# Optimization experiments

Hardware: AMD Instinct MI355X
Metric: run time of the kernel (lower is better)

Reference implementation:

```python
import jax, jax.numpy as jnp
import numpy as np

B, N_PTS, M_ROIS = 2, 8192, 2048
C_IN, O, H, NS = 128, 256, 4, 32
RADIUS = 1.6
BN_EPS = 1e-5
SCALE = 10.0  # point cloud extent


def setup_inputs() -> dict:
    key = jax.random.key(0)
    ks = jax.random.split(key, 20)
    f32 = jnp.float32
    Cg = C_IN + 3  # grouper concats relative xyz to features

    def kaiming(k, shape, fan_in):
        return jax.random.normal(k, shape, f32) * np.sqrt(2.0 / fan_in)

    inp = {
        "xyz": jax.random.uniform(ks[0], (B, N_PTS, 3), f32) * SCALE,
        "new_xyz": jax.random.uniform(ks[1], (B, M_ROIS, 3), f32) * SCALE,
        "features": jax.random.normal(ks[2], (B, C_IN, N_PTS), f32),
        # conv1d (kernel=1, no bias) weights, torch layout (out, in)
        "pos_w": kaiming(ks[3], (O, 3), 3),
        "key_w": kaiming(ks[4], (O, Cg), Cg),
        "val_w1": kaiming(ks[5], (O, Cg), Cg),
        "bn1_g": jnp.ones((O,), f32), "bn1_b": jnp.zeros((O,), f32),
        "val_w2": kaiming(ks[6], (O, O), O),
        "bn2_g": jnp.ones((O,), f32), "bn2_b": jnp.zeros((O,), f32),
        "attn_w": kaiming(ks[7], (H, O), O),
        # sigmoid-gated coefficient linears (no bias)
        "kc_w": kaiming(ks[8], (O, O), O),
        "qc_w": kaiming(ks[9], (O, O), O),
        "qkc_w": kaiming(ks[10], (O, O), O),
        "vc_w": kaiming(ks[11], (O, O), O),
        # cls/reg weight MLPs: Linear(O,O//2)+ReLU, Linear(O//2,1)+Sigmoid
        "cls_w1": kaiming(ks[12], (O // 2, O), O), "cls_b1": jnp.zeros((O // 2,), f32),
        "cls_w2": kaiming(ks[13], (1, O // 2), O // 2), "cls_b2": jnp.zeros((1,), f32),
        "reg_w1": kaiming(ks[14], (O // 2, O), O), "reg_b1": jnp.zeros((O // 2,), f32),
        "reg_w2": kaiming(ks[15], (1, O // 2), O // 2), "reg_b2": jnp.zeros((1,), f32),
    }
    return inp


def _bn(x, g, b):
    # eval-mode BatchNorm1d with running_mean=0, running_var=1 (init state)
    return g[None, :, None] * (x * (1.0 / np.sqrt(1.0 + BN_EPS))) + b[None, :, None]


def _conv1x1(w, x):  # (O,C) x (M,C,NS) -> (M,O,NS)
    return jnp.einsum('oc,mcn->mon', w, x)


def _ball_group(pts, q):
    # ball query: first NS points within RADIUS of each query (pad with first hit)
    n_tot = pts.shape[0]
    d2 = jnp.sum((q[:, None, :] - pts[None, :, :]) ** 2, axis=-1)  # (M, Ntot)
    order = jnp.where(d2 < RADIUS ** 2, jnp.arange(n_tot, dtype=jnp.int32), n_tot)
    neg_vals, idx = jax.lax.top_k(-order, NS)  # smallest indices among in-ball pts
    valid = (-neg_vals) < n_tot
    idx = jnp.where(valid, idx, idx[:, :1])  # pad with first neighbor
    has_any = valid[:, :1]
    idx = jnp.where(has_any, idx, 0)  # empty balls -> point 0
    return idx, ~has_any[:, 0]


def reference(xyz, new_xyz, features, pos_w, key_w, val_w1, bn1_g, bn1_b,
              val_w2, bn2_g, bn2_b, attn_w, kc_w, qc_w, qkc_w, vc_w,
              cls_w1, cls_b1, cls_w2, cls_b2, reg_w1, reg_b1, reg_w2, reg_b2):
    pts = xyz.reshape(-1, 3)                                   # (Ntot, 3)
    feats = features.transpose(0, 2, 1).reshape(-1, C_IN)      # (Ntot, C)
    q = new_xyz.reshape(-1, 3)                                 # (M, 3)

    idx, empty_mask = _ball_group(pts, q)                      # (M, NS)
    gx = pts[idx] - q[:, None, :]                              # relative xyz (M,NS,3)
    gxt = gx.transpose(0, 2, 1)                                # (M,3,NS)
    gf = jnp.concatenate([gx, feats[idx]], axis=-1).transpose(0, 2, 1)  # (M,C+3,NS)

    pos = jax.nn.relu(_conv1x1(pos_w, gxt))                    # (M,O,NS)
    key = jax.nn.relu(_conv1x1(key_w, gf))                     # (M,O,NS)
    v = jax.nn.relu(_bn(_conv1x1(val_w1, gf), bn1_g, bn1_b))
    val = jax.nn.relu(_bn(_conv1x1(val_w2, v), bn2_g, bn2_b))  # (M,O,NS)
    pos_key = pos * key

    sig = jax.nn.sigmoid
    v_c = sig(pos.mean(2) @ vc_w.T)                            # (M,O)
    q_c = sig(pos.mean(2) @ qc_w.T)
    k_c = sig(key.mean(2) @ kc_w.T)
    qk_c = sig(pos_key.mean(2) @ qkc_w.T)

    val = val + pos * v_c[:, :, None]
    attn_emb = pos * q_c[:, :, None] + key * k_c[:, :, None] + pos_key * qk_c[:, :, None]
    attn = jax.nn.softmax(jnp.einsum('ho,mon->mhn', attn_w, attn_emb), axis=-1)  # (M,H,NS)

    m = val.shape[0]
    vh = val.reshape(m, H, O // H, NS)
    new_features = jnp.einsum('mhdn,mhn->mhd', vh, attn).reshape(m, O)  # (M,O)

    def gate(x, w1, b1, w2, b2):
        return sig(jax.nn.relu(x @ w1.T + b1) @ w2.T + b2)

    cls_features = new_features * gate(new_features, cls_w1, cls_b1, cls_w2, cls_b2)
    reg_features = new_features * gate(new_features, reg_w1, reg_b1, reg_w2, reg_b2)
    return new_features, cls_features, reg_features
```

## Files before the change

kernel.cpp:

```cpp
#include <hip/hip_runtime.h>

#define DI __device__ __forceinline__

typedef __attribute__((ext_vector_type(8))) short bf16x8;
typedef __attribute__((ext_vector_type(4))) short s16x4;
typedef __attribute__((ext_vector_type(4))) float f32x4;

DI short f2bs(float x){ unsigned u = __float_as_uint(x);
  return (short)((u + 0x7FFF + ((u >> 16) & 1)) >> 16); }
DI float bs2f(short s){ return __uint_as_float(((unsigned)(unsigned short)s) << 16); }
DI f32x4 MFMA(bf16x8 a, bf16x8 b, f32x4 c){
  return __builtin_amdgcn_mfma_f32_16x16x32_bf16(a, b, c, 0, 0, 0);
}

constexpr int NP   = 8192;
constexpr int NTOT = 16384;
constexpr int M    = 4096;
constexpr int C    = 128;
constexpr int O    = 256;
constexpr int NS   = 32;
constexpr int H    = 4;
constexpr int GFS  = 136;
constexpr int VS   = 264;
constexpr float BNS = 0.99999500003749969f;

DI void copy64(short* __restrict__ dst, const short* __restrict__ src, int t){
  int row = t >> 2, off = (t & 3) * 64;
  const short* sp = src + row*VS + off;
  short* dp = dst + (size_t)row*O + off;
  #pragma unroll
  for(int j = 0; j < 8; j++)
    *(bf16x8*)(dp + j*8) = *(const bf16x8*)(sp + j*8);
}

__global__ __launch_bounds__(256) void k_transpose(const float* __restrict__ feat,
                                                   short* __restrict__ fT){
  __shared__ float tile[128][65];
  int blk = blockIdx.x;
  int b  = blk >> 7;
  int n0 = (blk & 127) << 6;
  int t = threadIdx.x;
  int nn = t & 63, c4 = t >> 6;
  const float* src = feat + (size_t)b * C * NP;
  for(int i = 0; i < 32; i++){
    int c = c4 * 32 + i;
    tile[c][nn] = src[(size_t)c * NP + n0 + nn];
  }
  __syncthreads();
  int c2 = t & 127, nb = t >> 7;
  for(int j = 0; j < 32; j++){
    int n = nb + j * 2;
    fT[((size_t)(b * NP + n0 + n)) * C + c2] = f2bs(tile[c2][n]);
  }
}

__global__ __launch_bounds__(256) void k_pack(
    const float* __restrict__ kw, const float* __restrict__ v1w,
    const float* __restrict__ v2w, const float* __restrict__ pw,
    const float* __restrict__ vcw, const float* __restrict__ qcw,
    const float* __restrict__ kcw, const float* __restrict__ qkcw,
    const float* __restrict__ cw1, const float* __restrict__ rw1,
    short* __restrict__ keyP, short* __restrict__ v1P,
    float* __restrict__ kgx, float* __restrict__ v1gx, float* __restrict__ pgx,
    short* __restrict__ v2b,
    short* __restrict__ gw,
    short* __restrict__ cw1b, short* __restrict__ rw1b)
{
  int i = blockIdx.x * 256 + threadIdx.x;
  if(i < O * C){
    int o = i >> 7, k = i & 127;
    keyP[i] = f2bs(kw[o*131 + 3 + k]);
    v1P[i]  = f2bs(v1w[o*131 + 3 + k]);
  }
  if(i < O){
    for(int j = 0; j < 3; j++){
      kgx [i*4+j] = kw [i*131 + j];
      v1gx[i*4+j] = v1w[i*131 + j];
      pgx [i*4+j] = pw [i*3 + j];
    }
    kgx[i*4+3] = 0.0f; v1gx[i*4+3] = 0.0f; pgx[i*4+3] = 0.0f;
  }
  if(i < O * O){
    v2b[i] = f2bs(v2w[i]);
    gw[0*O*O + i] = f2bs(vcw[i]);
    gw[1*O*O + i] = f2bs(qcw[i]);
    gw[2*O*O + i] = f2bs(kcw[i]);
    gw[3*O*O + i] = f2bs(qkcw[i]);
  }
  if(i < (O/2) * O){
    cw1b[i] = f2bs(cw1[i]);
    rw1b[i] = f2bs(rw1[i]);
  }
}

__global__ __launch_bounds__(64) void k_ballq(const float* __restrict__ xyz,
                                              const float* __restrict__ nxyz,
                                              int* __restrict__ idxo,
                                              float* __restrict__ gxo){
#pragma clang fp contract(off)
  int m = blockIdx.x;
  int lane = threadIdx.x;
  float qx = nxyz[m*3+0], qy = nxyz[m*3+1], qz = nxyz[m*3+2];
  __shared__ int sel[NS];
  int cnt = 0;
  for(int base = 0; base < NTOT; base += 64){
    int p = base + lane;
    float dx = qx - xyz[p*3+0], dy = qy - xyz[p*3+1], dz = qz - xyz[p*3+2];
    float d2 = dx*dx + dy*dy;
    d2 = d2 + dz*dz;
    bool pred = d2 < 2.56f;
    unsigned long long bal = __ballot(pred);
    if(pred){
      int pos = cnt + __popcll(bal & ((1ull << lane) - 1ull));
      if(pos < NS) sel[pos] = p;
    }
    cnt += __popcll(bal);
    if(cnt >= NS) break;
  }
  __syncthreads();
  if(lane < NS){
    int s = 0;
    if(cnt > 0) s = (lane < cnt) ? sel[lane] : sel[0];
    idxo[m*NS + lane] = s;
    gxo[(m*NS+lane)*3+0] = xyz[s*3+0] - qx;
    gxo[(m*NS+lane)*3+1] = xyz[s*3+1] - qy;
    gxo[(m*NS+lane)*3+2] = xyz[s*3+2] - qz;
  }
}

__global__ __launch_bounds__(256, 3) void k_conv(
    const short* __restrict__ fT,
    const short* __restrict__ keyP, const short* __restrict__ v1P,
    const float* __restrict__ kgx, const float* __restrict__ v1gx,
    const float* __restrict__ pgx,
    const short* __restrict__ v2b,
    const float* __restrict__ g1, const float* __restrict__ b1,
    const float* __restrict__ g2, const float* __restrict__ b2,
    const int* __restrict__ idxw, const float* __restrict__ gxw,
    short* __restrict__ keyo, short* __restrict__ valo,
    float* __restrict__ mPos, float* __restrict__ mKey, float* __restrict__ mPK,
    int q0)
{
  int lq2 = blockIdx.x, t = threadIdx.x;
  int w = t >> 6, l = t & 63;
  int col = l & 15, kq = l >> 4;
  int ro = w * 64;
  __shared__ __align__(16) short gf[64 * GFS];
  __shared__ __align__(16) short vst[64 * VS];
  __shared__ float gxs[64 * 4];
  __shared__ int  sel[64];
  int qg0 = q0 + lq2 * 2;
  if(t < 64){
    int qi = t >> 5, n = t & 31;
    int gq = qg0 + qi;
    sel[t] = idxw[gq*NS + n];
    gxs[t*4+0] = gxw[(gq*NS+n)*3+0];
    gxs[t*4+1] = gxw[(gq*NS+n)*3+1];
    gxs[t*4+2] = gxw[(gq*NS+n)*3+2];
    gxs[t*4+3] = 0.0f;
  }
  __syncthreads();
  for(int i = 0; i < 16; i++){
    int n = w*16 + i;
    int p = sel[n];
    *(unsigned*)&gf[n*GFS + l*2] = *(const unsigned*)(fT + (size_t)p * C + l*2);
  }
  __syncthreads();

  f32x4 acc[4][4];
  const f32x4 vzero = {0.0f, 0.0f, 0.0f, 0.0f};

  for(int mt=0;mt<4;mt++) for(int nt=0;nt<4;nt++) acc[mt][nt] = vzero;
  for(int ks = 0; ks < 4; ks++){
    bf16x8 bf[4];
    for(int nt=0;nt<4;nt++)
      bf[nt] = *(const bf16x8*)&gf[(nt*16+col)*GFS + ks*32 + kq*8];
    for(int mt = 0; mt < 4; mt++){
      bf16x8 a = *(const bf16x8*)(keyP + (size_t)(ro + mt*16 + col)*C + ks*32 + kq*8);
      for(int nt=0;nt<4;nt++) acc[mt][nt] = MFMA(a, bf[nt], acc[mt][nt]);
    }
  }
  for(int mt=0;mt<4;mt++){
    int o0 = ro + mt*16 + kq*4;
    f32x4 kg[4], pg[4];
    for(int r=0;r<4;r++){ kg[r] = *(const f32x4*)(kgx + (o0+r)*4);
                          pg[r] = *(const f32x4*)(pgx + (o0+r)*4); }
    for(int qi=0; qi<2; qi++){
      float sp[4]={0,0,0,0}, sk[4]={0,0,0,0}, spk[4]={0,0,0,0};
      for(int h=0; h<2; h++){
        int nt = qi*2 + h;
        int n  = nt*16 + col;
        float gx0 = gxs[n*4+0], gx1 = gxs[n*4+1], gx2 = gxs[n*4+2];
        s16x4 pk;
        for(int r=0;r<4;r++){
          float kk = fmaxf(acc[mt][nt][r] + kg[r][0]*gx0 + kg[r][1]*gx1 + kg[r][2]*gx2, 0.0f);
          float pv = fmaxf(pg[r][0]*gx0 + pg[r][1]*gx1 + pg[r][2]*gx2, 0.0f);
          pk[r] = f2bs(kk);
          sp[r] += pv; sk[r] += kk; spk[r] += pv*kk;
        }
        *(s16x4*)&vst[n*VS + o0] = pk;
      }
      for(int r=0;r<4;r++){
        float a = sp[r], b = sk[r], c = spk[r];
        for(int msk=1; msk<16; msk<<=1){
          a += __shfl_xor(a, msk); b += __shfl_xor(b, msk); c += __shfl_xor(c, msk);
        }
        if(col == 0){
          int lql = lq2*2 + qi;
          mPos[(size_t)lql*O + o0 + r] = a * 0.03125f;
          mKey[(size_t)lql*O + o0 + r] = b * 0.03125f;
          mPK [(size_t)lql*O + o0 + r] = c * 0.03125f;
        }
      }
    }
  }
  __syncthreads();
  copy64(keyo + (size_t)lq2*64*O, vst, t);

  for(int mt=0;mt<4;mt++) for(int nt=0;nt<4;nt++) acc[mt][nt] = vzero;
  for(int ks = 0; ks < 4; ks++){
    bf16x8 bf[4];
    for(int nt=0;nt<4;nt++)
      bf[nt] = *(const bf16x8*)&gf[(nt*16+col)*GFS + ks*32 + kq*8];
    for(int mt = 0; mt < 4; mt++){
      bf16x8 a = *(const bf16x8*)(v1P + (size_t)(ro + mt*16 + col)*C + ks*32 + kq*8);
      for(int nt=0;nt<4;nt++) acc[mt][nt] = MFMA(a, bf[nt], acc[mt][nt]);
    }
  }
  __syncthreads();
  for(int mt=0;mt<4;mt++){
    int o0 = ro + mt*16 + kq*4;
    f32x4 vg[4];
    float gg[4], bb[4];
    for(int r=0;r<4;r++){ vg[r] = *(const f32x4*)(v1gx + (o0+r)*4);
                          gg[r] = g1[o0+r]; bb[r] = b1[o0+r]; }
    for(int nt=0;nt<4;nt++){
      int n = nt*16 + col;
      float gx0 = gxs[n*4+0], gx1 = gxs[n*4+1], gx2 = gxs[n*4+2];
      s16x4 pk;
      for(int r=0;r<4;r++){
        float x = acc[mt][nt][r] + vg[r][0]*gx0 + vg[r][1]*gx1 + vg[r][2]*gx2;
        pk[r] = f2bs(fmaxf(gg[r]*(x * BNS) + bb[r], 0.0f));
      }
      *(s16x4*)&vst[n*VS + o0] = pk;
    }
  }
  __syncthreads();

  for(int mt=0;mt<4;mt++) for(int nt=0;nt<4;nt++) acc[mt][nt] = vzero;
  for(int ks = 0; ks < 8; ks++){
    bf16x8 bf[4];
    for(int nt=0;nt<4;nt++)
      bf[nt] = *(const bf16x8*)&vst[(nt*16+col)*VS + ks*32 + kq*8];
    for(int mt = 0; mt < 4; mt++){
      bf16x8 a = *(const bf16x8*)(v2b + (size_t)(ro + mt*16 + col)*O + ks*32 + kq*8);
      for(int nt=0;nt<4;nt++) acc[mt][nt] = MFMA(a, bf[nt], acc[mt][nt]);
    }
  }
  s16x4 valS[4][4];
  for(int mt=0;mt<4;mt++){
    int o0 = ro + mt*16 + kq*4;
    float gg[4], bb[4];
    for(int r=0;r<4;r++){ gg[r] = g2[o0+r]; bb[r] = b2[o0+r]; }
    for(int nt=0;nt<4;nt++)
      for(int r=0;r<4;r++)
        valS[mt][nt][r] = f2bs(fmaxf(gg[r]*(acc[mt][nt][r] * BNS) + bb[r], 0.0f));
  }
  __syncthreads();
  for(int mt=0;mt<4;mt++) for(int nt=0;nt<4;nt++){
    int n = nt*16 + col;
    *(s16x4*)&vst[n*VS + ro + mt*16 + kq*4] = valS[mt][nt];
  }
  __syncthreads();
  copy64(valo + (size_t)lq2*64*O, vst, t);
}

__global__ __launch_bounds__(256) void k_gates(
    const float* __restrict__ mPos, const float* __restrict__ mKey,
    const float* __restrict__ mPK, const short* __restrict__ gw,
    float* __restrict__ gates)
{
  int t = threadIdx.x, w = t >> 6, l = t & 63, col = l & 15, kq = l >> 4;
  int lq0 = blockIdx.x * 16;
  const float* A  = (w < 2) ? mPos : ((w == 2) ? mKey : mPK);
  const short* Wg = gw + (size_t)w * O * O;
  f32x4 acc[16];
  const f32x4 vzero = {0.0f,0.0f,0.0f,0.0f};
  for(int i=0;i<16;i++) acc[i] = vzero;
  for(int ks = 0; ks < 8; ks++){
    union { bf16x8 v; short e[8]; } u;
    const float* ap = A + (size_t)(lq0 + col)*O + ks*32 + kq*8;
    for(int j = 0; j < 8; j++) u.e[j] = f2bs(ap[j]);
    for(int nt = 0; nt < 16; nt++){
      bf16x8 bv = *(const bf16x8*)(Wg + (size_t)(nt*16 + col)*O + ks*32 + kq*8);
      acc[nt] = MFMA(u.v, bv, acc[nt]);
    }
  }
  for(int nt=0;nt<16;nt++) for(int r=0;r<4;r++){
    int lqq = lq0 + kq*4 + r;
    int oo = nt*16 + col;
    gates[((size_t)lqq*4 + w)*O + oo] = 1.0f / (1.0f + expf(-acc[nt][r]));
  }
}

__global__ __launch_bounds__(256) void k_attn(
    const short* __restrict__ keyw, const short* __restrict__ valw,
    const float* __restrict__ gxw, const float* __restrict__ posw,
    const float* __restrict__ attw, const float* __restrict__ gates,
    float* __restrict__ outNF, int q0)
{
  int lq = blockIdx.x, q = q0 + lq, t = threadIdx.x;
  __shared__ float emL[O * 33];
  __shared__ float attnL[H * NS];
  __shared__ float gxs[NS * 3];
  __shared__ float partial[256];
  if(t < 96) gxs[t] = gxw[q*96 + t];
  float vc  = gates[((size_t)lq*4 + 0)*O + t];
  float qc  = gates[((size_t)lq*4 + 1)*O + t];
  float kc  = gates[((size_t)lq*4 + 2)*O + t];
  float qkc = gates[((size_t)lq*4 + 3)*O + t];
  float pw0 = posw[t*3+0], pw1 = posw[t*3+1], pw2 = posw[t*3+2];
  __syncthreads();
  float posr[NS];
  for(int n = 0; n < NS; n++)
    posr[n] = fmaxf(pw0*gxs[n*3] + pw1*gxs[n*3+1] + pw2*gxs[n*3+2], 0.0f);
  for(int n = 0; n < NS; n++){
    float k = bs2f(keyw[((size_t)lq*NS + n)*O + t]);
    emL[t*33 + n] = posr[n]*qc + k*kc + posr[n]*k*qkc;
  }
  __syncthreads();
  {
    int idx = t & 127, h = idx >> 5, n = idx & 31, half = t >> 7;
    float s = 0;
    const float* aw = attw + h*O + half*128;
    for(int o = 0; o < 128; o++) s += aw[o] * emL[(half*128 + o)*33 + n];
    partial[t] = s;
  }
  __syncthreads();
  if(t < 128){
    int h = t >> 5, n = t & 31;
    float s = partial[t] + partial[t + 128];
    float mx = s;
    for(int msk=1; msk<32; msk<<=1) mx = fmaxf(mx, __shfl_xor(mx, msk));
    float e = expf(s - mx);
    float sum = e;
    for(int msk=1; msk<32; msk<<=1) sum += __shfl_xor(sum, msk);
    attnL[h*NS + n] = e / sum;
  }
  __syncthreads();
  int h = t >> 6;
  float nf = 0;
  for(int n = 0; n < NS; n++){
    float v = bs2f(valw[((size_t)lq*NS + n)*O + t]);
    nf += (v + posr[n]*vc) * attnL[h*NS + n];
  }
  outNF[(size_t)q*O + t] = nf;
}

__global__ __launch_bounds__(256) void k_fgate(
    const float* __restrict__ nf,
    const short* __restrict__ cw1b, const float* __restrict__ cb1,
    const float* __restrict__ cw2, const float* __restrict__ cb2,
    const short* __restrict__ rw1b, const float* __restrict__ rb1,
    const float* __restrict__ rw2, const float* __restrict__ rb2,
    float* __restrict__ outC, float* __restrict__ outR)
{
  int t = threadIdx.x, w = t >> 6, l = t & 63, col = l & 15, kq = l >> 4;
  int q0 = blockIdx.x * 64;
  __shared__ float sC[64], sR[64];
  f32x4 acc[16];
  const f32x4 vzero = {0.0f,0.0f,0.0f,0.0f};
  for(int i=0;i<16;i++) acc[i] = vzero;
  int arow = q0 + w*16 + col;
  for(int ks = 0; ks < 8; ks++){
    union { bf16x8 v; short e[8]; } u;
    const float* ap = nf + (size_t)arow*O + ks*32 + kq*8;
    for(int j = 0; j < 8; j++) u.e[j] = f2bs(ap[j]);
    for(int nt = 0; nt < 16; nt++){
      const short* W1 = (nt < 8) ? cw1b : rw1b;
      int j = (nt & 7)*16 + col;
      bf16x8 bv = *(const bf16x8*)(W1 + (size_t)j*O + ks*32 + kq*8);
      acc[nt] = MFMA(u.v, bv, acc[nt]);
    }
  }
  for(int r = 0; r < 4; r++){
    float pc = 0, pr = 0;
    for(int nt = 0; nt < 8; nt++){
      int j = nt*16 + col;
      pc += fmaxf(acc[nt][r] + cb1[j], 0.0f) * cw2[j];
    }
    for(int nt = 8; nt < 16; nt++){
      int j = (nt - 8)*16 + col;
      pr += fmaxf(acc[nt][r] + rb1[j], 0.0f) * rw2[j];
    }
    for(int msk=1; msk<16; msk<<=1){ pc += __shfl_xor(pc, msk); pr += __shfl_xor(pr, msk); }
    if(col == 0){
      int qq = w*16 + kq*4 + r;
      sC[qq] = 1.0f / (1.0f + expf(-(pc + cb2[0])));
      sR[qq] = 1.0f / (1.0f + expf(-(pr + rb2[0])));
    }
  }
  __syncthreads();
  for(int qq = 0; qq < 64; qq++){
    float nv = nf[(size_t)(q0 + qq)*O + t];
    outC[(size_t)(q0 + qq)*O + t] = nv * sC[qq];
    outR[(size_t)(q0 + qq)*O + t] = nv * sR[qq];
  }
}

extern "C" void kernel_launch(void* const* d_in, const int* in_sizes, int n_in,
                              void* d_out, int out_size, void* d_ws, size_t ws_size,
                              hipStream_t stream)
{
  const float* xyz  = (const float*)d_in[0];
  const float* nxyz = (const float*)d_in[1];
  const float* feat = (const float*)d_in[2];
  const float* posw = (const float*)d_in[3];
  const float* keyw = (const float*)d_in[4];
  const float* v1w  = (const float*)d_in[5];
  const float* bn1g = (const float*)d_in[6];
  const float* bn1b = (const float*)d_in[7];
  const float* v2w  = (const float*)d_in[8];
  const float* bn2g = (const float*)d_in[9];
  const float* bn2b = (const float*)d_in[10];
  const float* attw = (const float*)d_in[11];
  const float* kcw  = (const float*)d_in[12];
  const float* qcw  = (const float*)d_in[13];
  const float* qkcw = (const float*)d_in[14];
  const float* vcw  = (const float*)d_in[15];
  const float* cw1  = (const float*)d_in[16];
  const float* cb1  = (const float*)d_in[17];
  const float* cw2  = (const float*)d_in[18];
  const float* cb2  = (const float*)d_in[19];
  const float* rw1  = (const float*)d_in[20];
  const float* rb1  = (const float*)d_in[21];
  const float* rw2  = (const float*)d_in[22];
  const float* rb2  = (const float*)d_in[23];

  const size_t fixedB = 12000000;
  const size_t perQ   = 40960;
  int Q = 64;
  for(int cand : {4096, 2048, 1024, 512, 256, 128}){
    if(fixedB + (size_t)cand*perQ <= ws_size){ Q = cand; break; }
  }

  char* p = (char*)d_ws;
  auto alloc = [&](size_t bytes){ char* r = p; p += (bytes + 255) & ~size_t(255); return r; };
  short* fT    = (short*)alloc((size_t)NTOT*C*2);
  short* keyP  = (short*)alloc((size_t)O*C*2);
  short* v1P   = (short*)alloc((size_t)O*C*2);
  float* kgx   = (float*)alloc((size_t)O*4*4);
  float* v1gx  = (float*)alloc((size_t)O*4*4);
  float* pgx   = (float*)alloc((size_t)O*4*4);
  short* v2b   = (short*)alloc((size_t)O*O*2);
  short* gw    = (short*)alloc((size_t)4*O*O*2);
  short* cw1b  = (short*)alloc((size_t)(O/2)*O*2);
  short* rw1b  = (short*)alloc((size_t)(O/2)*O*2);
  int*   idxw  = (int*)  alloc((size_t)M*NS*4);
  float* gxw   = (float*)alloc((size_t)M*NS*3*4);
  short* keyo  = (short*)alloc((size_t)Q*NS*O*2);
  short* valo  = (short*)alloc((size_t)Q*NS*O*2);
  float* mPos  = (float*)alloc((size_t)Q*O*4);
  float* mKey  = (float*)alloc((size_t)Q*O*4);
  float* mPK   = (float*)alloc((size_t)Q*O*4);
  float* gates = (float*)alloc((size_t)Q*4*O*4);

  float* outNF = (float*)d_out;
  float* outC  = outNF + (size_t)M*O;
  float* outR  = outC  + (size_t)M*O;

  k_transpose<<<256, 256, 0, stream>>>(feat, fT);
  k_pack     <<<256, 256, 0, stream>>>(keyw, v1w, v2w, posw, vcw, qcw, kcw, qkcw, cw1, rw1,
                                       keyP, v1P, kgx, v1gx, pgx, v2b, gw, cw1b, rw1b);
  k_ballq    <<<M,   64,  0, stream>>>(xyz, nxyz, idxw, gxw);
  for(int q0 = 0; q0 < M; q0 += Q){
    k_conv  <<<Q/2,  256, 0, stream>>>(fT, keyP, v1P, kgx, v1gx, pgx, v2b,
                                       bn1g, bn1b, bn2g, bn2b,
                                       idxw, gxw, keyo, valo, mPos, mKey, mPK, q0);
    k_gates <<<Q/16, 256, 0, stream>>>(mPos, mKey, mPK, gw, gates);
    k_attn  <<<Q,    256, 0, stream>>>(keyo, valo, gxw, posw, attw, gates, outNF, q0);
  }
  k_fgate   <<<M/64, 256, 0, stream>>>(outNF, cw1b, cb1, cw2, cb2, rw1b, rb1, rw2, rb2, outC, outR);
}
```

Baseline: 438.1 us.

## Fuse conv, gate, attention and output-gating stages into one per-query-pair kernel

Merges k_conv, k_gates, k_attn and k_fgate into a single kernel that processes two queries per block. Key activations stay in registers, and means, gates, attention scores and new features stay in shared memory, so the bf16 key/value intermediates and gate buffers are never written to or read from global memory. The value-1 conv is computed first so its output can reuse the staging buffer. The gate and final MLP matmuls now run with only 2 useful columns out of 16 per MFMA, which wastes matrix throughput, and occupancy drops to 2 blocks per CU because of higher register and LDS use.

Result: slower. 570.8 us (+30.3%).

```diff
diff --git a/kernel.cpp b/kernel.cpp
--- a/kernel.cpp
+++ b/kernel.cpp
@@ -19,19 +19,9 @@
 constexpr int C    = 128;
 constexpr int O    = 256;
 constexpr int NS   = 32;
-constexpr int H    = 4;
 constexpr int GFS  = 136;
 constexpr int VS   = 264;
 constexpr float BNS = 0.99999500003749969f;
-
-DI void copy64(short* __restrict__ dst, const short* __restrict__ src, int t){
-  int row = t >> 2, off = (t & 3) * 64;
-  const short* sp = src + row*VS + off;
-  short* dp = dst + (size_t)row*O + off;
-  #pragma unroll
-  for(int j = 0; j < 8; j++)
-    *(bf16x8*)(dp + j*8) = *(const bf16x8*)(sp + j*8);
-}
 
 __global__ __launch_bounds__(256) void k_transpose(const float* __restrict__ feat,
                                                    short* __restrict__ fT){
@@ -64,7 +54,7 @@
     float* __restrict__ kgx, float* __restrict__ v1gx, float* __restrict__ pgx,
     short* __restrict__ v2b,
     short* __restrict__ gw,
-    short* __restrict__ cw1b, short* __restrict__ rw1b)
+    short* __restrict__ fgw)
 {
   int i = blockIdx.x * 256 + threadIdx.x;
   if(i < O * C){
@@ -86,10 +76,7 @@
     gw[1*O*O + i] = f2bs(qcw[i]);
     gw[2*O*O + i] = f2bs(kcw[i]);
     gw[3*O*O + i] = f2bs(qkcw[i]);
-  }
-  if(i < (O/2) * O){
-    cw1b[i] = f2bs(cw1[i]);
-    rw1b[i] = f2bs(rw1[i]);
+    fgw[i] = f2bs(i < 128*O ? cw1[i] : rw1[i - 128*O]);
   }
 }
 
@@ -128,18 +115,21 @@
   }
 }
 
-__global__ __launch_bounds__(256, 3) void k_conv(
+__global__ __launch_bounds__(256, 2) void k_fused(
     const short* __restrict__ fT,
     const short* __restrict__ keyP, const short* __restrict__ v1P,
     const float* __restrict__ kgx, const float* __restrict__ v1gx,
     const float* __restrict__ pgx,
-    const short* __restrict__ v2b,
+    const short* __restrict__ v2b, const short* __restrict__ gw,
+    const short* __restrict__ fgw, const float* __restrict__ attw,
     const float* __restrict__ g1, const float* __restrict__ b1,
     const float* __restrict__ g2, const float* __restrict__ b2,
+    const float* __restrict__ cb1, const float* __restrict__ cw2,
+    const float* __restrict__ cb2,
+    const float* __restrict__ rb1, const float* __restrict__ rw2,
+    const float* __restrict__ rb2,
     const int* __restrict__ idxw, const float* __restrict__ gxw,
-    short* __restrict__ keyo, short* __restrict__ valo,
-    float* __restrict__ mPos, float* __restrict__ mKey, float* __restrict__ mPK,
-    int q0)
+    float* __restrict__ outNF, float* __restrict__ outC, float* __restrict__ outR)
 {
   int lq2 = blockIdx.x, t = threadIdx.x;
   int w = t >> 6, l = t & 63;
@@ -149,7 +139,14 @@
   __shared__ __align__(16) short vst[64 * VS];
   __shared__ float gxs[64 * 4];
   __shared__ int  sel[64];
-  int qg0 = q0 + lq2 * 2;
+  __shared__ float attwL[4 * O];
+  __shared__ float meanL[3][2][O];
+  __shared__ float gatesL[4][2][O];
+  __shared__ float scoreP[4][4][64];
+  __shared__ float attnL[4][2][NS];
+  __shared__ float nfL[2][O];
+  __shared__ float pgsum[4][2];
+  int qg0 = lq2 * 2;
   if(t < 64){
     int qi = t >> 5, n = t & 31;
     int gq = qg0 + qi;
@@ -159,6 +156,7 @@
     gxs[t*4+2] = gxw[(gq*NS+n)*3+2];
     gxs[t*4+3] = 0.0f;
   }
+  for(int i = t; i < 4*O; i += 256) attwL[i] = attw[i];
   __syncthreads();
   for(int i = 0; i < 16; i++){
     int n = w*16 + i;
@@ -167,244 +165,240 @@
   }
   __syncthreads();
 
-  f32x4 acc[4][4];
   const f32x4 vzero = {0.0f, 0.0f, 0.0f, 0.0f};
 
-  for(int mt=0;mt<4;mt++) for(int nt=0;nt<4;nt++) acc[mt][nt] = vzero;
-  for(int ks = 0; ks < 4; ks++){
-    bf16x8 bf[4];
-    for(int nt=0;nt<4;nt++)
-      bf[nt] = *(const bf16x8*)&gf[(nt*16+col)*GFS + ks*32 + kq*8];
-    for(int mt = 0; mt < 4; mt++){
-      bf16x8 a = *(const bf16x8*)(keyP + (size_t)(ro + mt*16 + col)*C + ks*32 + kq*8);
-      for(int nt=0;nt<4;nt++) acc[mt][nt] = MFMA(a, bf[nt], acc[mt][nt]);
-    }
-  }
-  for(int mt=0;mt<4;mt++){
-    int o0 = ro + mt*16 + kq*4;
-    f32x4 kg[4], pg[4];
-    for(int r=0;r<4;r++){ kg[r] = *(const f32x4*)(kgx + (o0+r)*4);
-                          pg[r] = *(const f32x4*)(pgx + (o0+r)*4); }
-    for(int qi=0; qi<2; qi++){
-      float sp[4]={0,0,0,0}, sk[4]={0,0,0,0}, spk[4]={0,0,0,0};
-      for(int h=0; h<2; h++){
-        int nt = qi*2 + h;
-        int n  = nt*16 + col;
+  {
+    f32x4 acc[4][4];
+    for(int mt=0;mt<4;mt++) for(int nt=0;nt<4;nt++) acc[mt][nt] = vzero;
+    for(int ks = 0; ks < 4; ks++){
+      bf16x8 bf[4];
+      for(int nt=0;nt<4;nt++)
+        bf[nt] = *(const bf16x8*)&gf[(nt*16+col)*GFS + ks*32 + kq*8];
+      for(int mt = 0; mt < 4; mt++){
+        bf16x8 a = *(const bf16x8*)(v1P + (size_t)(ro + mt*16 + col)*C + ks*32 + kq*8);
+        for(int nt=0;nt<4;nt++) acc[mt][nt] = MFMA(a, bf[nt], acc[mt][nt]);
+      }
+    }
+    for(int mt=0;mt<4;mt++){
+      int o0 = ro + mt*16 + kq*4;
+      f32x4 vg[4];
+      float gg[4], bb[4];
+      for(int r=0;r<4;r++){ vg[r] = *(const f32x4*)(v1gx + (o0+r)*4);
+                            gg[r] = g1[o0+r]; bb[r] = b1[o0+r]; }
+      for(int nt=0;nt<4;nt++){
+        int n = nt*16 + col;
         float gx0 = gxs[n*4+0], gx1 = gxs[n*4+1], gx2 = gxs[n*4+2];
         s16x4 pk;
         for(int r=0;r<4;r++){
-          float kk = fmaxf(acc[mt][nt][r] + kg[r][0]*gx0 + kg[r][1]*gx1 + kg[r][2]*gx2, 0.0f);
-          float pv = fmaxf(pg[r][0]*gx0 + pg[r][1]*gx1 + pg[r][2]*gx2, 0.0f);
-          pk[r] = f2bs(kk);
-          sp[r] += pv; sk[r] += kk; spk[r] += pv*kk;
+          float x = acc[mt][nt][r] + vg[r][0]*gx0 + vg[r][1]*gx1 + vg[r][2]*gx2;
+          pk[r] = f2bs(fmaxf(gg[r]*(x * BNS) + bb[r], 0.0f));
         }
         *(s16x4*)&vst[n*VS + o0] = pk;
       }
+    }
+  }
+
+  f32x4 accK[4][4];
+  {
+    for(int mt=0;mt<4;mt++) for(int nt=0;nt<4;nt++) accK[mt][nt] = vzero;
+    for(int ks = 0; ks < 4; ks++){
+      bf16x8 bf[4];
+      for(int nt=0;nt<4;nt++)
+        bf[nt] = *(const bf16x8*)&gf[(nt*16+col)*GFS + ks*32 + kq*8];
+      for(int mt = 0; mt < 4; mt++){
+        bf16x8 a = *(const bf16x8*)(keyP + (size_t)(ro + mt*16 + col)*C + ks*32 + kq*8);
+        for(int nt=0;nt<4;nt++) accK[mt][nt] = MFMA(a, bf[nt], accK[mt][nt]);
+      }
+    }
+    for(int mt=0;mt<4;mt++){
+      int o0 = ro + mt*16 + kq*4;
+      f32x4 kg[4], pg[4];
+      for(int r=0;r<4;r++){ kg[r] = *(const f32x4*)(kgx + (o0+r)*4);
+                            pg[r] = *(const f32x4*)(pgx + (o0+r)*4); }
+      for(int qi=0; qi<2; qi++){
+        float sp[4]={0,0,0,0}, sk[4]={0,0,0,0}, spk[4]={0,0,0,0};
+        for(int h=0; h<2; h++){
+          int nt = qi*2 + h;
+          int n  = nt*16 + col;
+          float gx0 = gxs[n*4+0], gx1 = gxs[n*4+1], gx2 = gxs[n*4+2];
+          for(int r=0;r<4;r++){
+            float kk = fmaxf(accK[mt][nt][r] + kg[r][0]*gx0 + kg[r][1]*gx1 + kg[r][2]*gx2, 0.0f);
+            accK[mt][nt][r] = kk;
+            float pv = fmaxf(pg[r][0]*gx0 + pg[r][1]*gx1 + pg[r][2]*gx2, 0.0f);
+            sp[r] += pv; sk[r] += kk; spk[r] += pv*kk;
+          }
+        }
+        for(int r=0;r<4;r++){
+          float a = sp[r], b = sk[r], c = spk[r];
+          for(int msk=1; msk<16; msk<<=1){
+            a += __shfl_xor(a, msk); b += __shfl_xor(b, msk); c += __shfl_xor(c, msk);
+          }
+          if(col == 0){
+            meanL[0][qi][o0+r] = a * 0.03125f;
+            meanL[1][qi][o0+r] = b * 0.03125f;
+            meanL[2][qi][o0+r] = c * 0.03125f;
+          }
+        }
+      }
+    }
+  }
+  __syncthreads();
+
+  {
+    int mty = (w < 2) ? 0 : ((w == 2) ? 1 : 2);
+    f32x4 ag[16];
+    for(int i=0;i<16;i++) ag[i] = vzero;
+    for(int ks = 0; ks < 8; ks++){
+      union { bf16x8 v; short e[8]; } u;
+      for(int j = 0; j < 8; j++){
+        int k = ks*32 + kq*8 + j;
+        u.e[j] = (col < 2) ? f2bs(meanL[mty][col][k]) : (short)0;
+      }
+      for(int mt16 = 0; mt16 < 16; mt16++){
+        bf16x8 a = *(const bf16x8*)(gw + (size_t)w*O*O + (size_t)(mt16*16 + col)*O + ks*32 + kq*8);
+        ag[mt16] = MFMA(a, u.v, ag[mt16]);
+      }
+    }
+    if(col < 2){
+      for(int mt16=0;mt16<16;mt16++) for(int r=0;r<4;r++){
+        int oo = mt16*16 + kq*4 + r;
+        gatesL[w][col][oo] = 1.0f / (1.0f + expf(-ag[mt16][r]));
+      }
+    }
+  }
+  __syncthreads();
+
+  {
+    float sc[4][4];
+    for(int h=0;h<4;h++) for(int nt=0;nt<4;nt++) sc[h][nt] = 0.0f;
+    for(int mt=0;mt<4;mt++){
+      int o0 = ro + mt*16 + kq*4;
+      f32x4 pg[4];
+      float aw[4][4], qcv[2][4], kcv[2][4], qkv[2][4];
       for(int r=0;r<4;r++){
-        float a = sp[r], b = sk[r], c = spk[r];
-        for(int msk=1; msk<16; msk<<=1){
-          a += __shfl_xor(a, msk); b += __shfl_xor(b, msk); c += __shfl_xor(c, msk);
-        }
-        if(col == 0){
-          int lql = lq2*2 + qi;
-          mPos[(size_t)lql*O + o0 + r] = a * 0.03125f;
-          mKey[(size_t)lql*O + o0 + r] = b * 0.03125f;
-          mPK [(size_t)lql*O + o0 + r] = c * 0.03125f;
-        }
-      }
-    }
-  }
-  __syncthreads();
-  copy64(keyo + (size_t)lq2*64*O, vst, t);
-
-  for(int mt=0;mt<4;mt++) for(int nt=0;nt<4;nt++) acc[mt][nt] = vzero;
-  for(int ks = 0; ks < 4; ks++){
-    bf16x8 bf[4];
-    for(int nt=0;nt<4;nt++)
-      bf[nt] = *(const bf16x8*)&gf[(nt*16+col)*GFS + ks*32 + kq*8];
-    for(int mt = 0; mt < 4; mt++){
-      bf16x8 a = *(const bf16x8*)(v1P + (size_t)(ro + mt*16 + col)*C + ks*32 + kq*8);
-      for(int nt=0;nt<4;nt++) acc[mt][nt] = MFMA(a, bf[nt], acc[mt][nt]);
-    }
-  }
-  __syncthreads();
-  for(int mt=0;mt<4;mt++){
-    int o0 = ro + mt*16 + kq*4;
-    f32x4 vg[4];
-    float gg[4], bb[4];
-    for(int r=0;r<4;r++){ vg[r] = *(const f32x4*)(v1gx + (o0+r)*4);
-                          gg[r] = g1[o0+r]; bb[r] = b1[o0+r]; }
-    for(int nt=0;nt<4;nt++){
-      int n = nt*16 + col;
-      float gx0 = gxs[n*4+0], gx1 = gxs[n*4+1], gx2 = gxs[n*4+2];
-      s16x4 pk;
-      for(int r=0;r<4;r++){
-        float x = acc[mt][nt][r] + vg[r][0]*gx0 + vg[r][1]*gx1 + vg[r][2]*gx2;
-        pk[r] = f2bs(fmaxf(gg[r]*(x * BNS) + bb[r], 0.0f));
-      }
-      *(s16x4*)&vst[n*VS + o0] = pk;
-    }
-  }
-  __syncthreads();
-
-  for(int mt=0;mt<4;mt++) for(int nt=0;nt<4;nt++) acc[mt][nt] = vzero;
-  for(int ks = 0; ks < 8; ks++){
-    bf16x8 bf[4];
-    for(int nt=0;nt<4;nt++)
-      bf[nt] = *(const bf16x8*)&vst[(nt*16+col)*VS + ks*32 + kq*8];
-    for(int mt = 0; mt < 4; mt++){
-      bf16x8 a = *(const bf16x8*)(v2b + (size_t)(ro + mt*16 + col)*O + ks*32 + kq*8);
-      for(int nt=0;nt<4;nt++) acc[mt][nt] = MFMA(a, bf[nt], acc[mt][nt]);
-    }
-  }
-  s16x4 valS[4][4];
-  for(int mt=0;mt<4;mt++){
-    int o0 = ro + mt*16 + kq*4;
-    float gg[4], bb[4];
-    for(int r=0;r<4;r++){ gg[r] = g2[o0+r]; bb[r] = b2[o0+r]; }
-    for(int nt=0;nt<4;nt++)
-      for(int r=0;r<4;r++)
-        valS[mt][nt][r] = f2bs(fmaxf(gg[r]*(acc[mt][nt][r] * BNS) + bb[r], 0.0f));
-  }
-  __syncthreads();
-  for(int mt=0;mt<4;mt++) for(int nt=0;nt<4;nt++){
-    int n = nt*16 + col;
-    *(s16x4*)&vst[n*VS + ro + mt*16 + kq*4] = valS[mt][nt];
-  }
-  __syncthreads();
-  copy64(valo + (size_t)lq2*64*O, vst, t);
-}
-
-__global__ __launch_bounds__(256) void k_gates(
-    const float* __restrict__ mPos, const float* __restrict__ mKey,
-    const float* __restrict__ mPK, const short* __restrict__ gw,
-    float* __restrict__ gates)
-{
-  int t = threadIdx.x, w = t >> 6, l = t & 63, col = l & 15, kq = l >> 4;
-  int lq0 = blockIdx.x * 16;
-  const float* A  = (w < 2) ? mPos : ((w == 2) ? mKey : mPK);
-  const short* Wg = gw + (size_t)w * O * O;
-  f32x4 acc[16];
-  const f32x4 vzero = {0.0f,0.0f,0.0f,0.0f};
-  for(int i=0;i<16;i++) acc[i] = vzero;
-  for(int ks = 0; ks < 8; ks++){
-    union { bf16x8 v; short e[8]; } u;
-    const float* ap = A + (size_t)(lq0 + col)*O + ks*32 + kq*8;
-    for(int j = 0; j < 8; j++) u.e[j] = f2bs(ap[j]);
-    for(int nt = 0; nt < 16; nt++){
-      bf16x8 bv = *(const bf16x8*)(Wg + (size_t)(nt*16 + col)*O + ks*32 + kq*8);
-      acc[nt] = MFMA(u.v, bv, acc[nt]);
-    }
-  }
-  for(int nt=0;nt<16;nt++) for(int r=0;r<4;r++){
-    int lqq = lq0 + kq*4 + r;
-    int oo = nt*16 + col;
-    gates[((size_t)lqq*4 + w)*O + oo] = 1.0f / (1.0f + expf(-acc[nt][r]));
-  }
-}
-
-__global__ __launch_bounds__(256) void k_attn(
-    const short* __restrict__ keyw, const short* __restrict__ valw,
-    const float* __restrict__ gxw, const float* __restrict__ posw,
-    const float* __restrict__ attw, const float* __restrict__ gates,
-    float* __restrict__ outNF, int q0)
-{
-  int lq = blockIdx.x, q = q0 + lq, t = threadIdx.x;
-  __shared__ float emL[O * 33];
-  __shared__ float attnL[H * NS];
-  __shared__ float gxs[NS * 3];
-  __shared__ float partial[256];
-  if(t < 96) gxs[t] = gxw[q*96 + t];
-  float vc  = gates[((size_t)lq*4 + 0)*O + t];
-  float qc  = gates[((size_t)lq*4 + 1)*O + t];
-  float kc  = gates[((size_t)lq*4 + 2)*O + t];
-  float qkc = gates[((size_t)lq*4 + 3)*O + t];
-  float pw0 = posw[t*3+0], pw1 = posw[t*3+1], pw2 = posw[t*3+2];
-  __syncthreads();
-  float posr[NS];
-  for(int n = 0; n < NS; n++)
-    posr[n] = fmaxf(pw0*gxs[n*3] + pw1*gxs[n*3+1] + pw2*gxs[n*3+2], 0.0f);
-  for(int n = 0; n < NS; n++){
-    float k = bs2f(keyw[((size_t)lq*NS + n)*O + t]);
-    emL[t*33 + n] = posr[n]*qc + k*kc + posr[n]*k*qkc;
-  }
-  __syncthreads();
-  {
-    int idx = t & 127, h = idx >> 5, n = idx & 31, half = t >> 7;
-    float s = 0;
-    const float* aw = attw + h*O + half*128;
-    for(int o = 0; o < 128; o++) s += aw[o] * emL[(half*128 + o)*33 + n];
-    partial[t] = s;
-  }
-  __syncthreads();
-  if(t < 128){
-    int h = t >> 5, n = t & 31;
-    float s = partial[t] + partial[t + 128];
+        pg[r] = *(const f32x4*)(pgx + (o0+r)*4);
+        for(int h=0;h<4;h++) aw[h][r] = attwL[h*O + o0 + r];
+        for(int qi=0;qi<2;qi++){
+          qcv[qi][r] = gatesL[1][qi][o0+r];
+          kcv[qi][r] = gatesL[2][qi][o0+r];
+          qkv[qi][r] = gatesL[3][qi][o0+r];
+        }
+      }
+      for(int nt=0;nt<4;nt++){
+        int qi = nt >> 1;
+        int n  = nt*16 + col;
+        float gx0 = gxs[n*4+0], gx1 = gxs[n*4+1], gx2 = gxs[n*4+2];
+        for(int r=0;r<4;r++){
+          float pos = fmaxf(pg[r][0]*gx0 + pg[r][1]*gx1 + pg[r][2]*gx2, 0.0f);
+          float key = accK[mt][nt][r];
+          float em  = pos*qcv[qi][r] + key*kcv[qi][r] + pos*key*qkv[qi][r];
+          for(int h=0;h<4;h++) sc[h][nt] += aw[h][r]*em;
+        }
+      }
+    }
+    for(int h=0;h<4;h++) for(int nt=0;nt<4;nt++){
+      float v = sc[h][nt];
+      v += __shfl_xor(v, 16); v += __shfl_xor(v, 32);
+      if(kq == 0) scoreP[w][h][nt*16 + col] = v;
+    }
+  }
+  __syncthreads();
+
+  {
+    float s = scoreP[0][w][l] + scoreP[1][w][l] + scoreP[2][w][l] + scoreP[3][w][l];
     float mx = s;
     for(int msk=1; msk<32; msk<<=1) mx = fmaxf(mx, __shfl_xor(mx, msk));
     float e = expf(s - mx);
-    float sum = e;
-    for(int msk=1; msk<32; msk<<=1) sum += __shfl_xor(sum, msk);
-    attnL[h*NS + n] = e / sum;
-  }
-  __syncthreads();
-  int h = t >> 6;
-  float nf = 0;
-  for(int n = 0; n < NS; n++){
-    float v = bs2f(valw[((size_t)lq*NS + n)*O + t]);
-    nf += (v + posr[n]*vc) * attnL[h*NS + n];
-  }
-  outNF[(size_t)q*O + t] = nf;
-}
-
-__global__ __launch_bounds__(256) void k_fgate(
-    const float* __restrict__ nf,
-    const short* __restrict__ cw1b, const float* __restrict__ cb1,
-    const float* __restrict__ cw2, const float* __restrict__ cb2,
-    const short* __restrict__ rw1b, const float* __restrict__ rb1,
-    const float* __restrict__ rw2, const float* __restrict__ rb2,
-    float* __restrict__ outC, float* __restrict__ outR)
-{
-  int t = threadIdx.x, w = t >> 6, l = t & 63, col = l & 15, kq = l >> 4;
-  int q0 = blockIdx.x * 64;
-  __shared__ float sC[64], sR[64];
-  f32x4 acc[16];
-  const f32x4 vzero = {0.0f,0.0f,0.0f,0.0f};
-  for(int i=0;i<16;i++) acc[i] = vzero;
-  int arow = q0 + w*16 + col;
-  for(int ks = 0; ks < 8; ks++){
-    union { bf16x8 v; short e[8]; } u;
-    const float* ap = nf + (size_t)arow*O + ks*32 + kq*8;
-    for(int j = 0; j < 8; j++) u.e[j] = f2bs(ap[j]);
-    for(int nt = 0; nt < 16; nt++){
-      const short* W1 = (nt < 8) ? cw1b : rw1b;
-      int j = (nt & 7)*16 + col;
-      bf16x8 bv = *(const bf16x8*)(W1 + (size_t)j*O + ks*32 + kq*8);
-      acc[nt] = MFMA(u.v, bv, acc[nt]);
-    }
-  }
-  for(int r = 0; r < 4; r++){
-    float pc = 0, pr = 0;
-    for(int nt = 0; nt < 8; nt++){
-      int j = nt*16 + col;
-      pc += fmaxf(acc[nt][r] + cb1[j], 0.0f) * cw2[j];
-    }
-    for(int nt = 8; nt < 16; nt++){
-      int j = (nt - 8)*16 + col;
-      pr += fmaxf(acc[nt][r] + rb1[j], 0.0f) * rw2[j];
-    }
-    for(int msk=1; msk<16; msk<<=1){ pc += __shfl_xor(pc, msk); pr += __shfl_xor(pr, msk); }
-    if(col == 0){
-      int qq = w*16 + kq*4 + r;
-      sC[qq] = 1.0f / (1.0f + expf(-(pc + cb2[0])));
-      sR[qq] = 1.0f / (1.0f + expf(-(pr + rb2[0])));
-    }
-  }
-  __syncthreads();
-  for(int qq = 0; qq < 64; qq++){
-    float nv = nf[(size_t)(q0 + qq)*O + t];
-    outC[(size_t)(q0 + qq)*O + t] = nv * sC[qq];
-    outR[(size_t)(q0 + qq)*O + t] = nv * sR[qq];
+    float su = e;
+    for(int msk=1; msk<32; msk<<=1) su += __shfl_xor(su, msk);
+    attnL[w][l>>5][l&31] = e / su;
+  }
+  __syncthreads();
+
+  {
+    f32x4 acc[4][4];
+    for(int mt=0;mt<4;mt++) for(int nt=0;nt<4;nt++) acc[mt][nt] = vzero;
+    for(int ks = 0; ks < 8; ks++){
+      bf16x8 bf[4];
+      for(int nt=0;nt<4;nt++)
+        bf[nt] = *(const bf16x8*)&vst[(nt*16+col)*VS + ks*32 + kq*8];
+      for(int mt = 0; mt < 4; mt++){
+        bf16x8 a = *(const bf16x8*)(v2b + (size_t)(ro + mt*16 + col)*O + ks*32 + kq*8);
+        for(int nt=0;nt<4;nt++) acc[mt][nt] = MFMA(a, bf[nt], acc[mt][nt]);
+      }
+    }
+    for(int mt=0;mt<4;mt++){
+      int o0 = ro + mt*16 + kq*4;
+      f32x4 pg[4];
+      float gg[4], bb[4], vcv[2][4];
+      for(int r=0;r<4;r++){
+        pg[r] = *(const f32x4*)(pgx + (o0+r)*4);
+        gg[r] = g2[o0+r]; bb[r] = b2[o0+r];
+        vcv[0][r] = gatesL[0][0][o0+r];
+        vcv[1][r] = gatesL[0][1][o0+r];
+      }
+      float nf2[2][4];
+      for(int qi=0;qi<2;qi++) for(int r=0;r<4;r++) nf2[qi][r] = 0.0f;
+      for(int nt=0;nt<4;nt++){
+        int qi = nt >> 1;
+        int nn = (nt&1)*16 + col;
+        int n  = nt*16 + col;
+        float gx0 = gxs[n*4+0], gx1 = gxs[n*4+1], gx2 = gxs[n*4+2];
+        float at = attnL[w][qi][nn];
+        for(int r=0;r<4;r++){
+          float val = fmaxf(gg[r]*(acc[mt][nt][r] * BNS) + bb[r], 0.0f);
+          float pos = fmaxf(pg[r][0]*gx0 + pg[r][1]*gx1 + pg[r][2]*gx2, 0.0f);
+          nf2[qi][r] += (val + pos*vcv[qi][r]) * at;
+        }
+      }
+      for(int qi=0;qi<2;qi++) for(int r=0;r<4;r++){
+        float v = nf2[qi][r];
+        v += __shfl_xor(v, 1); v += __shfl_xor(v, 2);
+        v += __shfl_xor(v, 4); v += __shfl_xor(v, 8);
+        if(col == 0) nfL[qi][o0+r] = v;
+      }
+    }
+  }
+  __syncthreads();
+
+  {
+    f32x4 ac[4];
+    for(int i=0;i<4;i++) ac[i] = vzero;
+    for(int ks = 0; ks < 8; ks++){
+      union { bf16x8 v; short e[8]; } u;
+      for(int j = 0; j < 8; j++){
+        int k = ks*32 + kq*8 + j;
+        u.e[j] = (col < 2) ? f2bs(nfL[col][k]) : (short)0;
+      }
+      for(int mt = 0; mt < 4; mt++){
+        bf16x8 a = *(const bf16x8*)(fgw + (size_t)(w*64 + mt*16 + col)*O + ks*32 + kq*8);
+        ac[mt] = MFMA(a, u.v, ac[mt]);
+      }
+    }
+    bool cls = (w < 2);
+    const float* b1p = cls ? cb1 : rb1;
+    const float* w2p = cls ? cw2 : rw2;
+    int jbase = (cls ? w : (w - 2)) * 64;
+    float pp = 0.0f;
+    for(int mt=0;mt<4;mt++) for(int r=0;r<4;r++){
+      int j = jbase + mt*16 + kq*4 + r;
+      pp += fmaxf(ac[mt][r] + b1p[j], 0.0f) * w2p[j];
+    }
+    pp += __shfl_xor(pp, 16); pp += __shfl_xor(pp, 32);
+    if(kq == 0 && col < 2) pgsum[w][col] = pp;
+  }
+  __syncthreads();
+
+  {
+    for(int qi = 0; qi < 2; qi++){
+      float sC = 1.0f / (1.0f + expf(-(pgsum[0][qi] + pgsum[1][qi] + cb2[0])));
+      float sR = 1.0f / (1.0f + expf(-(pgsum[2][qi] + pgsum[3][qi] + rb2[0])));
+      int q = qg0 + qi;
+      float nv = nfL[qi][t];
+      outNF[(size_t)q*O + t] = nv;
+      outC [(size_t)q*O + t] = nv * sC;
+      outR [(size_t)q*O + t] = nv * sR;
+    }
   }
 }
 
@@ -437,13 +431,6 @@
   const float* rw2  = (const float*)d_in[22];
   const float* rb2  = (const float*)d_in[23];
 
-  const size_t fixedB = 12000000;
-  const size_t perQ   = 40960;
-  int Q = 64;
-  for(int cand : {4096, 2048, 1024, 512, 256, 128}){
-    if(fixedB + (size_t)cand*perQ <= ws_size){ Q = cand; break; }
-  }
-
   char* p = (char*)d_ws;
   auto alloc = [&](size_t bytes){ char* r = p; p += (bytes + 255) & ~size_t(255); return r; };
   short* fT    = (short*)alloc((size_t)NTOT*C*2);
@@ -454,16 +441,9 @@
   float* pgx   = (float*)alloc((size_t)O*4*4);
   short* v2b   = (short*)alloc((size_t)O*O*2);
   short* gw    = (short*)alloc((size_t)4*O*O*2);
-  short* cw1b  = (short*)alloc((size_t)(O/2)*O*2);
-  short* rw1b  = (short*)alloc((size_t)(O/2)*O*2);
+  short* fgw   = (short*)alloc((size_t)O*O*2);
   int*   idxw  = (int*)  alloc((size_t)M*NS*4);
   float* gxw   = (float*)alloc((size_t)M*NS*3*4);
-  short* keyo  = (short*)alloc((size_t)Q*NS*O*2);
-  short* valo  = (short*)alloc((size_t)Q*NS*O*2);
-  float* mPos  = (float*)alloc((size_t)Q*O*4);
-  float* mKey  = (float*)alloc((size_t)Q*O*4);
-  float* mPK   = (float*)alloc((size_t)Q*O*4);
-  float* gates = (float*)alloc((size_t)Q*4*O*4);
 
   float* outNF = (float*)d_out;
   float* outC  = outNF + (size_t)M*O;
@@ -471,14 +451,10 @@
 
   k_transpose<<<256, 256, 0, stream>>>(feat, fT);
   k_pack     <<<256, 256, 0, stream>>>(keyw, v1w, v2w, posw, vcw, qcw, kcw, qkcw, cw1, rw1,
-                                       keyP, v1P, kgx, v1gx, pgx, v2b, gw, cw1b, rw1b);
+                                       keyP, v1P, kgx, v1gx, pgx, v2b, gw, fgw);
   k_ballq    <<<M,   64,  0, stream>>>(xyz, nxyz, idxw, gxw);
-  for(int q0 = 0; q0 < M; q0 += Q){
-    k_conv  <<<Q/2,  256, 0, stream>>>(fT, keyP, v1P, kgx, v1gx, pgx, v2b,
+  k_fused    <<<M/2, 256, 0, stream>>>(fT, keyP, v1P, kgx, v1gx, pgx, v2b, gw, fgw, attw,
                                        bn1g, bn1b, bn2g, bn2b,
-                                       idxw, gxw, keyo, valo, mPos, mKey, mPK, q0);
-    k_gates <<<Q/16, 256, 0, stream>>>(mPos, mKey, mPK, gw, gates);
-    k_attn  <<<Q,    256, 0, stream>>>(keyo, valo, gxw, posw, attw, gates, outNF, q0);
-  }
-  k_fgate   <<<M/64, 256, 0, stream>>>(outNF, cw1b, cb1, cw2, cb2, rw1b, rb1, rw2, rb2, outC, outR);
-}
+                                       cb1, cw2, cb2, rb1, rw2, rb2,
+                                       idxw, gxw, outNF, outC, outR);
+}
```
